# Kernel optimization log

Hardware: AMD Instinct MI355X
Metric: run time of the kernel (lower is better)

## Reference

```python
import jax, jax.numpy as jnp
import numpy as np

N = 50000      # nodes
E = 800000     # edges (before self loops)
IN = 128       # in_channels
C = 64         # out_channels per head
H = 4          # heads (both layers)
NEG_SLOPE = 0.2


def setup_inputs():
    key = jax.random.key(0)
    ks = jax.random.split(key, 14)
    nrm = lambda k, sh, s: jax.random.normal(k, sh, dtype=jnp.float32) * s
    x = nrm(ks[0], (N, IN), 1.0)
    edge_index = jax.random.randint(ks[1], (2, E), 0, N, dtype=jnp.int32)
    batch = jnp.zeros((N,), dtype=jnp.int32)
    edge_attr = jax.random.uniform(ks[2], (E, 1), dtype=jnp.float32)
    # layer 1 params (PyG GATConv: lin, att_src, att_dst, lin_edge, att_edge, bias)
    W1 = nrm(ks[3], (IN, H * C), 1.0 / np.sqrt(IN))
    We1 = nrm(ks[4], (1, H * C), 1.0)
    att_s1 = nrm(ks[5], (H, C), 1.0 / np.sqrt(C))
    att_d1 = nrm(ks[6], (H, C), 1.0 / np.sqrt(C))
    att_e1 = nrm(ks[7], (H, C), 1.0 / np.sqrt(C))
    b1 = jnp.zeros((H * C,), dtype=jnp.float32)
    # layer 2 params (in = H*C = 256)
    W2 = nrm(ks[8], (H * C, H * C), 1.0 / np.sqrt(H * C))
    We2 = nrm(ks[9], (1, H * C), 1.0)
    att_s2 = nrm(ks[10], (H, C), 1.0 / np.sqrt(C))
    att_d2 = nrm(ks[11], (H, C), 1.0 / np.sqrt(C))
    att_e2 = nrm(ks[12], (H, C), 1.0 / np.sqrt(C))
    b2 = jnp.zeros((H * C,), dtype=jnp.float32)
    return dict(x=x, edge_index=edge_index, batch=batch, edge_attr=edge_attr,
                W1=W1, We1=We1, att_s1=att_s1, att_d1=att_d1, att_e1=att_e1, b1=b1,
                W2=W2, We2=We2, att_s2=att_s2, att_d2=att_d2, att_e2=att_e2, b2=b2)


def gat_layer(h_in, src, dst, e_attr, W, We, att_s, att_d, att_e, b):
    n = h_in.shape[0]
    h = (h_in @ W).reshape(n, H, C)                      # [N,H,C]
    a_src = jnp.einsum('nhc,hc->nh', h, att_s)           # [N,H]
    a_dst = jnp.einsum('nhc,hc->nh', h, att_d)
    e = (e_attr @ We).reshape(-1, H, C)                  # [E',H,C]
    a_edge = jnp.einsum('ehc,hc->eh', e, att_e)          # [E',H]
    alpha = jax.nn.leaky_relu(a_src[src] + a_dst[dst] + a_edge, NEG_SLOPE)
    # softmax over edges grouped by destination node
    amax = jax.ops.segment_max(alpha, dst, num_segments=n)
    amax = jnp.where(jnp.isfinite(amax), amax, 0.0)
    ex = jnp.exp(alpha - amax[dst])
    denom = jax.ops.segment_sum(ex, dst, num_segments=n)
    a = ex / (denom[dst] + 1e-16)                        # [E',H]
    out = jax.ops.segment_sum(a[:, :, None] * h[src], dst, num_segments=n)
    return out.reshape(n, H * C) + b


def reference(x, edge_index, batch, edge_attr,
              W1, We1, att_s1, att_d1, att_e1, b1,
              W2, We2, att_s2, att_d2, att_e2, b2):
    n = x.shape[0]
    # PyG GATConv default: add self loops, self-loop edge_attr = mean fill
    loop = jnp.arange(n, dtype=edge_index.dtype)
    src = jnp.concatenate([edge_index[0], loop])
    dst = jnp.concatenate([edge_index[1], loop])
    ea_fill = jnp.broadcast_to(edge_attr.mean(axis=0, keepdims=True), (n, edge_attr.shape[1]))
    ea = jnp.concatenate([edge_attr, ea_fill], axis=0)
    h1 = gat_layer(x, src, dst, ea, W1, We1, att_s1, att_d1, att_e1, b1)
    h2 = gat_layer(h1, src, dst, ea, W2, We2, att_s2, att_d2, att_e2, b2)
    return h2
```

## Files before the change

kernel.cpp:

```cpp
#include <hip/hip_runtime.h>

#define NEG_SLOPE 0.2f

typedef __attribute__((ext_vector_type(8))) short bf16x8;
typedef __attribute__((ext_vector_type(4))) float f32x4;

__device__ inline unsigned short f2bf(float x) {
  unsigned int u = __float_as_uint(x);
  u += 0x7fffu + ((u >> 16) & 1u);
  return (unsigned short)(u >> 16);
}

__device__ inline unsigned fkey(float x) {
  unsigned u = __float_as_uint(x);
  return (u >> 31) ? ~u : (u | 0x80000000u);
}
__device__ inline float fkey_dec(unsigned k) {
  unsigned u = (k & 0x80000000u) ? (k ^ 0x80000000u) : ~k;
  return __uint_as_float(u);
}


__global__ void hist_kernel(const int* __restrict__ ei, int* __restrict__ counts,
                            int E, int Etot) {
  int e = blockIdx.x * blockDim.x + threadIdx.x;
  if (e >= Etot) return;
  int d = (e < E) ? ei[E + e] : (e - E);
  atomicAdd(&counts[d], 1);
}

__global__ void mean_kernel(const float* __restrict__ ea, float* __restrict__ acc, int E) {
  int i = blockIdx.x * blockDim.x + threadIdx.x;
  float s = 0.f;
  for (; i < E; i += gridDim.x * blockDim.x) s += ea[i];
#pragma unroll
  for (int off = 1; off < 64; off <<= 1) s += __shfl_xor(s, off, 64);
  if ((threadIdx.x & 63) == 0) atomicAdd(acc, s);
}

__global__ void scan_blocksum(const int* __restrict__ counts, int* __restrict__ bsum, int Nn) {
  int base = blockIdx.x * 4096 + threadIdx.x * 16;
  int s = 0;
#pragma unroll
  for (int i = 0; i < 16; i++) { int idx = base + i; if (idx < Nn) s += counts[idx]; }
#pragma unroll
  for (int off = 1; off < 64; off <<= 1) s += __shfl_xor(s, off, 64);
  __shared__ int ws_[4];
  if ((threadIdx.x & 63) == 0) ws_[threadIdx.x >> 6] = s;
  __syncthreads();
  if (threadIdx.x == 0) bsum[blockIdx.x] = ws_[0] + ws_[1] + ws_[2] + ws_[3];
}

__global__ void scan_offsets(int* bsum, int nb, int* rowptrN,
                             const float* meanacc, float* meanv, int E) {
  if (threadIdx.x == 0 && blockIdx.x == 0) {
    int acc = 0;
    for (int i = 0; i < nb; i++) { int v = bsum[i]; bsum[i] = acc; acc += v; }
    *rowptrN = acc;
    *meanv = *meanacc / (float)E;
  }
}

__global__ void scan_final(const int* __restrict__ counts, const int* __restrict__ bsum,
                           int* __restrict__ rowptr, int* __restrict__ cursor, int Nn) {
  int base = blockIdx.x * 4096 + threadIdx.x * 16;
  int v[16]; int s = 0;
#pragma unroll
  for (int i = 0; i < 16; i++) { int idx = base + i; v[i] = (idx < Nn) ? counts[idx] : 0; s += v[i]; }
  int lane = threadIdx.x & 63, wv = threadIdx.x >> 6;
  int incl = s;
#pragma unroll
  for (int off = 1; off < 64; off <<= 1) {
    int y = __shfl_up(incl, off, 64);
    if (lane >= off) incl += y;
  }
  __shared__ int wtot[4];
  if (lane == 63) wtot[wv] = incl;
  __syncthreads();
  int run = bsum[blockIdx.x] + incl - s;
  for (int i = 0; i < wv; i++) run += wtot[i];
  for (int i = 0; i < 16; i++) {
    int idx = base + i;
    if (idx < Nn) { rowptr[idx] = run; cursor[idx] = run; }
    run += v[i];
  }
}

__global__ void scatter_kernel(const int* __restrict__ ei, const float* __restrict__ eattr,
                               const float* __restrict__ meanv,
                               int* __restrict__ cursor, int2* __restrict__ epack,
                               int E, int Etot) {
  int e = blockIdx.x * blockDim.x + threadIdx.x;
  if (e >= Etot) return;
  int d, s; float ea;
  if (e < E) { d = ei[E + e]; s = ei[e]; ea = eattr[e]; }
  else       { d = e - E;     s = e - E; ea = meanv[0]; }
  int pos = atomicAdd(&cursor[d], 1);
  epack[pos] = make_int2(s, __float_as_int(ea));
}

__global__ void weatt_kernel(const float* __restrict__ We1, const float* __restrict__ atte1,
                             const float* __restrict__ We2, const float* __restrict__ atte2,
                             float* __restrict__ weatt1, float* __restrict__ weatt2) {
  int t = threadIdx.x;
  const float* We = (t < 256) ? We1 : We2;
  const float* at = (t < 256) ? atte1 : atte2;
  float* wo = (t < 256) ? weatt1 : weatt2;
  int i = t & 255;
  float p = We[i] * at[i];
#pragma unroll
  for (int off = 1; off < 64; off <<= 1) p += __shfl_xor(p, off, 64);
  if ((i & 63) == 0) wo[i >> 6] = p;
}

__global__ void wtrans_kernel(const float* __restrict__ W1, unsigned short* __restrict__ Wt1,
                              const float* __restrict__ W2, unsigned short* __restrict__ Wt2) {
  int b = blockIdx.x;
  const float* W; unsigned short* Wt; int K, t;
  if (b < 128) { W = W1; Wt = Wt1; K = 128; t = b * 256 + threadIdx.x; }
  else         { W = W2; Wt = Wt2; K = 256; t = (b - 128) * 256 + threadIdx.x; }
  int n = t & 255, k = t >> 8;
  if (k >= K) return;
  Wt[(size_t)n * K + k] = f2bf(W[(size_t)k * 256 + n]);
}


template <int AF32>
__device__ inline bf16x8 load_a_row(const void* Ain, int gr, int K, int kpos, int M) {
  bf16x8 v = {};
  if (gr < M) {
    if (AF32) {
      const float* src = (const float*)Ain + (size_t)gr * K + kpos;
      float4 f0 = *(const float4*)src;
      float4 f1 = *(const float4*)(src + 4);
      v[0] = (short)f2bf(f0.x); v[1] = (short)f2bf(f0.y);
      v[2] = (short)f2bf(f0.z); v[3] = (short)f2bf(f0.w);
      v[4] = (short)f2bf(f1.x); v[5] = (short)f2bf(f1.y);
      v[6] = (short)f2bf(f1.z); v[7] = (short)f2bf(f1.w);
    } else {
      v = *(const bf16x8*)((const unsigned short*)Ain + (size_t)gr * K + kpos);
    }
  }
  return v;
}

#define CS_STRIDE 264

template <int AF32>
__global__ __launch_bounds__(512) void gemm_att(const void* __restrict__ Ain,
                                                const unsigned short* __restrict__ Wt,
                                                unsigned short* __restrict__ Hb,
                                                const float* __restrict__ atts,
                                                const float* __restrict__ attd,
                                                float* __restrict__ asrc,
                                                float* __restrict__ adst,
                                                unsigned* __restrict__ gmaxk,
                                                int M, int K) {
  __shared__ __align__(16) short smem[(128 + 256) * 64];
  short* As = smem;
  short* Bs = smem + 128 * 64;
  short* Cs = smem;
  const int tid = threadIdx.x;
  const int lane = tid & 63, wv = tid >> 6;
  const int wm = wv >> 2, wn = wv & 3;
  const int l15 = lane & 15, l4 = lane >> 4;
  const int bm = blockIdx.x * 128;

  const int r0 = tid >> 3, kc = (tid & 7) * 8;
  const int nbB = tid >> 3, cB = (tid & 7) * 8;

  f32x4 acc[4][4] = {};
  bf16x8 ra0, ra1, rb0, rb1, rb2, rb3;

#define GLOAD_TILE(K0, A0, A1, B0, B1, B2, B3)                                 \
  {                                                                            \
    A0 = load_a_row<AF32>(Ain, bm + r0, K, (K0) + kc, M);                      \
    A1 = load_a_row<AF32>(Ain, bm + r0 + 64, K, (K0) + kc, M);                 \
    B0 = *(const bf16x8*)&Wt[(size_t)(nbB +   0) * K + (K0) + cB];             \
    B1 = *(const bf16x8*)&Wt[(size_t)(nbB +  64) * K + (K0) + cB];             \
    B2 = *(const bf16x8*)&Wt[(size_t)(nbB + 128) * K + (K0) + cB];             \
    B3 = *(const bf16x8*)&Wt[(size_t)(nbB + 192) * K + (K0) + cB];             \
  }

  GLOAD_TILE(0, ra0, ra1, rb0, rb1, rb2, rb3)

  for (int k0 = 0; k0 < K; k0 += 64) {
    *(bf16x8*)&As[((r0) * 64 + kc) ^ ((r0 & 7) << 3)] = ra0;
    *(bf16x8*)&As[((r0 + 64) * 64 + kc) ^ ((r0 & 7) << 3)] = ra1;
    *(bf16x8*)&Bs[((nbB) * 64 + cB) ^ ((nbB & 7) << 3)] = rb0;
    *(bf16x8*)&Bs[((nbB + 64) * 64 + cB) ^ ((nbB & 7) << 3)] = rb1;
    *(bf16x8*)&Bs[((nbB + 128) * 64 + cB) ^ ((nbB & 7) << 3)] = rb2;
    *(bf16x8*)&Bs[((nbB + 192) * 64 + cB) ^ ((nbB & 7) << 3)] = rb3;
    __syncthreads();

    bool more = (k0 + 64 < K);
    bf16x8 na0, na1, nb0, nb1, nb2, nb3;
    if (more) GLOAD_TILE(k0 + 64, na0, na1, nb0, nb1, nb2, nb3)

    bf16x8 af[4][2], bfr[4][2];
#pragma unroll
    for (int rt = 0; rt < 4; rt++)
#pragma unroll
      for (int ks = 0; ks < 2; ks++) {
        int row = wm * 64 + rt * 16 + l15;
        int kb = l4 * 8 + ks * 32;
        af[rt][ks] = *(const bf16x8*)&As[(row * 64 + kb) ^ ((row & 7) << 3)];
      }
#pragma unroll
    for (int ct = 0; ct < 4; ct++)
#pragma unroll
      for (int ks = 0; ks < 2; ks++) {
        int n = wn * 64 + ct * 16 + l15;
        int kb = l4 * 8 + ks * 32;
        bfr[ct][ks] = *(const bf16x8*)&Bs[(n * 64 + kb) ^ ((n & 7) << 3)];
      }
#pragma unroll
    for (int rt = 0; rt < 4; rt++)
#pragma unroll
      for (int ct = 0; ct < 4; ct++)
#pragma unroll
        for (int ks = 0; ks < 2; ks++)
          acc[rt][ct] = __builtin_amdgcn_mfma_f32_16x16x32_bf16(
              af[rt][ks], bfr[ct][ks], acc[rt][ct], 0, 0, 0);
    __syncthreads();

    if (more) { ra0 = na0; ra1 = na1; rb0 = nb0; rb1 = nb1; rb2 = nb2; rb3 = nb3; }
  }
#undef GLOAD_TILE

  float s_att[4], d_att[4];
#pragma unroll
  for (int ct = 0; ct < 4; ct++) {
    s_att[ct] = atts[wn * 64 + ct * 16 + l15];
    d_att[ct] = attd[wn * 64 + ct * 16 + l15];
  }
  float ps[4][4] = {}, pd[4][4] = {};
#pragma unroll
  for (int rt = 0; rt < 4; rt++)
#pragma unroll
    for (int ct = 0; ct < 4; ct++)
#pragma unroll
      for (int i = 0; i < 4; i++) {
        float v = acc[rt][ct][i];
        ps[rt][i] = fmaf(v, s_att[ct], ps[rt][i]);
        pd[rt][i] = fmaf(v, d_att[ct], pd[rt][i]);
      }

  for (int h = 0; h < 2; h++) {
    __syncthreads();
    if (wm == h) {
#pragma unroll
      for (int rt = 0; rt < 4; rt++)
#pragma unroll
        for (int ct = 0; ct < 4; ct++)
#pragma unroll
          for (int i = 0; i < 4; i++) {
            int lrow = rt * 16 + l4 * 4 + i;
            Cs[lrow * CS_STRIDE + wn * 64 + ct * 16 + l15] = f2bf(acc[rt][ct][i]);
          }
    }
    __syncthreads();
    int row = tid >> 3, seg = tid & 7;
    int gr = bm + h * 64 + row;
    if (gr < M) {
      const short* srcr = &Cs[row * CS_STRIDE + seg * 32];
      unsigned short* dstr = &Hb[(size_t)gr * 256 + seg * 32];
#pragma unroll
      for (int k = 0; k < 4; k++)
        *(uint4*)&dstr[k * 8] = *(const uint4*)&srcr[k * 8];
    }
  }

#pragma unroll
  for (int rt = 0; rt < 4; rt++)
#pragma unroll
    for (int i = 0; i < 4; i++) {
#pragma unroll
      for (int off = 1; off < 16; off <<= 1) {
        ps[rt][i] += __shfl_xor(ps[rt][i], off, 64);
        pd[rt][i] += __shfl_xor(pd[rt][i], off, 64);
      }
    }
  float mx = ps[0][0];
#pragma unroll
  for (int rt = 0; rt < 4; rt++)
#pragma unroll
    for (int i = 0; i < 4; i++) mx = fmaxf(mx, ps[rt][i]);
  mx = fmaxf(mx, __shfl_xor(mx, 16, 64));
  mx = fmaxf(mx, __shfl_xor(mx, 32, 64));
  if (lane == 0) atomicMax(&gmaxk[wn * 32], fkey(mx));
  if (l15 == 0) {
#pragma unroll
    for (int rt = 0; rt < 4; rt++)
#pragma unroll
      for (int i = 0; i < 4; i++) {
        int gr = bm + wm * 64 + rt * 16 + l4 * 4 + i;
        if (gr < M) {
          asrc[gr * 4 + wn] = ps[rt][i];
          adst[gr * 4 + wn] = pd[rt][i];
        }
      }
  }
}


#define AGG_PH1(CNT)                                                        \
  int src = 0; float w = 0.f;                                               \
  if (il < (CNT)) {                                                         \
    int2 e = epack[p + il];                                                 \
    float al = fmaf(__int_as_float(e.y), wa, asrc[e.x * 4 + hh] + ad);      \
    al = fmaxf(al, NEG_SLOPE * al);                                         \
    w = __expf(al - b);                                                     \
    src = e.x;                                                              \
  }                                                                         \
  ssum += w;

#define AGG_GATHER(i)                                                       \
  {                                                                         \
    int sl = (i) | hb16;                                                    \
    int si = __shfl(src, sl, 64);                                           \
    float wi = __shfl(w, sl, 64);                                           \
    uint2 hv = *(const uint2*)&Hb[(size_t)((unsigned)si * 256u + co)];      \
    acc.x = fmaf(wi, __uint_as_float(hv.x << 16), acc.x);                   \
    acc.y = fmaf(wi, __uint_as_float(hv.x & 0xffff0000u), acc.y);           \
    acc.z = fmaf(wi, __uint_as_float(hv.y << 16), acc.z);                   \
    acc.w = fmaf(wi, __uint_as_float(hv.y & 0xffff0000u), acc.w);           \
  }

template <int OUTBF>
__global__ __launch_bounds__(256) void gat_agg(const unsigned short* __restrict__ Hb,
                                               const float* __restrict__ asrc,
                                               const float* __restrict__ adst,
                                               const int* __restrict__ rowptr,
                                               const int2* __restrict__ epack,
                                               const float* __restrict__ weatt,
                                               const unsigned* __restrict__ gmaxk,
                                               const float* __restrict__ bias,
                                               unsigned short* __restrict__ outb,
                                               float* __restrict__ outf, int Nn) {
  int wid = (blockIdx.x * blockDim.x + threadIdx.x) >> 6;
  int lane = threadIdx.x & 63;
  if (wid >= Nn) return;
  int beg = rowptr[wid], end = rowptr[wid + 1];
  int hh = lane >> 4;
  int il = lane & 15;
  int hb16 = lane & 48;
  float wa = weatt[hh];
  float ad = adst[wid * 4 + hh];
  float braw = ad + fkey_dec(gmaxk[hh * 32]) + fmaxf(wa, 0.f);
  float b = fmaxf(braw, NEG_SLOPE * braw);
  unsigned co = (unsigned)lane * 4u;

  float ssum = 0.f;
  float4 acc = {0.f, 0.f, 0.f, 0.f};

  int p = beg;
  for (; p + 16 <= end; p += 16) {
    AGG_PH1(16)
#pragma unroll
    for (int i = 0; i < 16; i++) AGG_GATHER(i)
  }
  int cnt = end - p;
  if (cnt > 0) {
    AGG_PH1(cnt)
    for (int i = 0; i < cnt; i++) AGG_GATHER(i)
  }

#pragma unroll
  for (int off = 1; off < 16; off <<= 1) ssum += __shfl_xor(ssum, off, 64);

  float inv = 1.f / (ssum + 1e-16f);
  float4 b4 = *(const float4*)&bias[co];
  float4 r;
  r.x = fmaf(acc.x, inv, b4.x);
  r.y = fmaf(acc.y, inv, b4.y);
  r.z = fmaf(acc.z, inv, b4.z);
  r.w = fmaf(acc.w, inv, b4.w);
  if (OUTBF) {
    unsigned lo = (unsigned)f2bf(r.x) | ((unsigned)f2bf(r.y) << 16);
    unsigned hi = (unsigned)f2bf(r.z) | ((unsigned)f2bf(r.w) << 16);
    *(uint2*)&outb[(size_t)wid * 256 + co] = make_uint2(lo, hi);
  } else {
    *(float4*)&outf[(size_t)wid * 256 + co] = r;
  }
}


extern "C" void kernel_launch(void* const* d_in, const int* in_sizes, int n_in,
                              void* d_out, int out_size, void* d_ws, size_t ws_size,
                              hipStream_t stream) {
  (void)n_in; (void)out_size; (void)ws_size;
  const float* x     = (const float*)d_in[0];
  const int*   ei    = (const int*)d_in[1];
  const float* eattr = (const float*)d_in[3];
  const float* W1    = (const float*)d_in[4];
  const float* We1   = (const float*)d_in[5];
  const float* atts1 = (const float*)d_in[6];
  const float* attd1 = (const float*)d_in[7];
  const float* atte1 = (const float*)d_in[8];
  const float* b1    = (const float*)d_in[9];
  const float* W2    = (const float*)d_in[10];
  const float* We2   = (const float*)d_in[11];
  const float* atts2 = (const float*)d_in[12];
  const float* attd2 = (const float*)d_in[13];
  const float* atte2 = (const float*)d_in[14];
  const float* b2    = (const float*)d_in[15];
  float* out = (float*)d_out;

  const int Nn   = in_sizes[0] / 128;
  const int E    = in_sizes[1] / 2;
  const int Etot = E + Nn;

  char* p = (char*)d_ws;
  auto alloc = [&](size_t bytes) { void* r = (void*)p; p += (bytes + 255) & ~(size_t)255; return r; };
  int*      counts  = (int*)alloc((size_t)Nn * 4);
  float*    meanacc = (float*)alloc(4);
  unsigned* gmaxk1  = (unsigned*)alloc(512);
  unsigned* gmaxk2  = (unsigned*)alloc(512);
  char* zero_end = p;
  int*   rowptr  = (int*)alloc((size_t)(Nn + 1) * 4);
  int*   cursor  = (int*)alloc((size_t)Nn * 4);
  int2*  epack   = (int2*)alloc((size_t)Etot * 8);
  int*   bsum    = (int*)alloc(64 * 4);
  float* meanv   = (float*)alloc(4);
  float* weatt1  = (float*)alloc(16);
  float* weatt2  = (float*)alloc(16);
  float* asrc    = (float*)alloc((size_t)Nn * 4 * 4);
  float* adst    = (float*)alloc((size_t)Nn * 4 * 4);
  unsigned short* hbuf = (unsigned short*)alloc((size_t)Nn * 256 * 2);
  unsigned short* h1b  = (unsigned short*)alloc((size_t)Nn * 256 * 2);
  unsigned short* Wt1  = (unsigned short*)alloc((size_t)256 * 128 * 2);
  unsigned short* Wt2  = (unsigned short*)alloc((size_t)256 * 256 * 2);

  const int NB = (Nn + 4095) / 4096;

  hipMemsetAsync(counts, 0, (size_t)(zero_end - (char*)counts), stream);

  hist_kernel<<<(Etot + 255) / 256, 256, 0, stream>>>(ei, counts, E, Etot);
  mean_kernel<<<512, 256, 0, stream>>>(eattr, meanacc, E);
  scan_blocksum<<<NB, 256, 0, stream>>>(counts, bsum, Nn);
  scan_offsets<<<1, 64, 0, stream>>>(bsum, NB, rowptr + Nn, meanacc, meanv, E);
  scan_final<<<NB, 256, 0, stream>>>(counts, bsum, rowptr, cursor, Nn);
  scatter_kernel<<<(Etot + 255) / 256, 256, 0, stream>>>(ei, eattr, meanv, cursor, epack, E, Etot);
  weatt_kernel<<<1, 512, 0, stream>>>(We1, atte1, We2, atte2, weatt1, weatt2);
  wtrans_kernel<<<384, 256, 0, stream>>>(W1, Wt1, W2, Wt2);

  const int gemmBlocks = (Nn + 127) / 128;
  const int nodeBlocks = (Nn + 3) / 4;

  gemm_att<1><<<gemmBlocks, 512, 0, stream>>>(x, Wt1, hbuf, atts1, attd1,
                                              asrc, adst, gmaxk1, Nn, 128);
  gat_agg<1><<<nodeBlocks, 256, 0, stream>>>(hbuf, asrc, adst, rowptr, epack,
                                             weatt1, gmaxk1, b1, h1b, nullptr, Nn);
  gemm_att<0><<<gemmBlocks, 512, 0, stream>>>(h1b, Wt2, hbuf, atts2, attd2,
                                              asrc, adst, gmaxk2, Nn, 256);
  gat_agg<0><<<nodeBlocks, 256, 0, stream>>>(hbuf, asrc, adst, rowptr, epack,
                                             weatt2, gmaxk2, b2, nullptr, out, Nn);
}
```

Baseline: 344.3 us.

## Merge scan kernels into single-block scan, fold weatt into wtrans, reduce gmax atomics

Replaces the three-kernel counts scan plus the mean finalisation with one 1024-thread single-block kernel, which also sums per-block mean partials instead of using a float atomic. The weatt computation is folded into an extra block of the weight-transpose kernel. In the GEMM, the attention-logit reduction moves before the C-tile store, and per-block max is combined in shared memory so only four atomics are issued per block. Together these cut kernel launches and atomic traffic, at the cost of a serial single-block scan over 50k counts.

```diff
diff --git a/kernel.cpp b/kernel.cpp
--- a/kernel.cpp
+++ b/kernel.cpp
@@ -29,60 +29,59 @@
   atomicAdd(&counts[d], 1);
 }
 
-__global__ void mean_kernel(const float* __restrict__ ea, float* __restrict__ acc, int E) {
+__global__ void mean_kernel(const float* __restrict__ ea, float* __restrict__ part, int E) {
   int i = blockIdx.x * blockDim.x + threadIdx.x;
   float s = 0.f;
   for (; i < E; i += gridDim.x * blockDim.x) s += ea[i];
 #pragma unroll
   for (int off = 1; off < 64; off <<= 1) s += __shfl_xor(s, off, 64);
-  if ((threadIdx.x & 63) == 0) atomicAdd(acc, s);
-}
-
-__global__ void scan_blocksum(const int* __restrict__ counts, int* __restrict__ bsum, int Nn) {
-  int base = blockIdx.x * 4096 + threadIdx.x * 16;
-  int s = 0;
-#pragma unroll
-  for (int i = 0; i < 16; i++) { int idx = base + i; if (idx < Nn) s += counts[idx]; }
-#pragma unroll
-  for (int off = 1; off < 64; off <<= 1) s += __shfl_xor(s, off, 64);
-  __shared__ int ws_[4];
+  __shared__ float ws_[4];
   if ((threadIdx.x & 63) == 0) ws_[threadIdx.x >> 6] = s;
   __syncthreads();
-  if (threadIdx.x == 0) bsum[blockIdx.x] = ws_[0] + ws_[1] + ws_[2] + ws_[3];
-}
-
-__global__ void scan_offsets(int* bsum, int nb, int* rowptrN,
-                             const float* meanacc, float* meanv, int E) {
-  if (threadIdx.x == 0 && blockIdx.x == 0) {
-    int acc = 0;
-    for (int i = 0; i < nb; i++) { int v = bsum[i]; bsum[i] = acc; acc += v; }
-    *rowptrN = acc;
-    *meanv = *meanacc / (float)E;
-  }
-}
-
-__global__ void scan_final(const int* __restrict__ counts, const int* __restrict__ bsum,
-                           int* __restrict__ rowptr, int* __restrict__ cursor, int Nn) {
-  int base = blockIdx.x * 4096 + threadIdx.x * 16;
-  int v[16]; int s = 0;
-#pragma unroll
-  for (int i = 0; i < 16; i++) { int idx = base + i; v[i] = (idx < Nn) ? counts[idx] : 0; s += v[i]; }
-  int lane = threadIdx.x & 63, wv = threadIdx.x >> 6;
+  if (threadIdx.x == 0) part[blockIdx.x] = ws_[0] + ws_[1] + ws_[2] + ws_[3];
+}
+
+__global__ __launch_bounds__(1024) void scan_all(const int* __restrict__ counts,
+                                                 int* __restrict__ rowptr,
+                                                 int* __restrict__ cursor,
+                                                 const float* __restrict__ meanpart,
+                                                 float* __restrict__ meanv,
+                                                 int Nn, int E, int npart) {
+  __shared__ int wsum[16];
+  __shared__ float fsum[16];
+  int t = threadIdx.x, lane = t & 63, wv = t >> 6;
+  float f = (t < npart) ? meanpart[t] : 0.f;
+#pragma unroll
+  for (int off = 1; off < 64; off <<= 1) f += __shfl_xor(f, off, 64);
+  if (lane == 0) fsum[wv] = f;
+  const int CH = (Nn + 1023) >> 10;
+  int base = t * CH;
+  int lim = base + CH < Nn ? base + CH : Nn;
+  int s = 0;
+  for (int i = base; i < lim; i++) s += counts[i];
   int incl = s;
 #pragma unroll
   for (int off = 1; off < 64; off <<= 1) {
     int y = __shfl_up(incl, off, 64);
     if (lane >= off) incl += y;
   }
-  __shared__ int wtot[4];
-  if (lane == 63) wtot[wv] = incl;
+  if (lane == 63) wsum[wv] = incl;
   __syncthreads();
-  int run = bsum[blockIdx.x] + incl - s;
-  for (int i = 0; i < wv; i++) run += wtot[i];
-  for (int i = 0; i < 16; i++) {
-    int idx = base + i;
-    if (idx < Nn) { rowptr[idx] = run; cursor[idx] = run; }
-    run += v[i];
+  if (t == 0) {
+    int acc = 0;
+    for (int i = 0; i < 16; i++) { int x = wsum[i]; wsum[i] = acc; acc += x; }
+    rowptr[Nn] = acc;
+    float fa = 0.f;
+    for (int i = 0; i < 16; i++) fa += fsum[i];
+    *meanv = fa / (float)E;
+  }
+  __syncthreads();
+  int run = wsum[wv] + incl - s;
+  for (int i = base; i < lim; i++) {
+    int c = counts[i];
+    rowptr[i] = run;
+    cursor[i] = run;
+    run += c;
   }
 }
 
@@ -99,23 +98,26 @@
   epack[pos] = make_int2(s, __float_as_int(ea));
 }
 
-__global__ void weatt_kernel(const float* __restrict__ We1, const float* __restrict__ atte1,
-                             const float* __restrict__ We2, const float* __restrict__ atte2,
-                             float* __restrict__ weatt1, float* __restrict__ weatt2) {
-  int t = threadIdx.x;
-  const float* We = (t < 256) ? We1 : We2;
-  const float* at = (t < 256) ? atte1 : atte2;
-  float* wo = (t < 256) ? weatt1 : weatt2;
-  int i = t & 255;
-  float p = We[i] * at[i];
-#pragma unroll
-  for (int off = 1; off < 64; off <<= 1) p += __shfl_xor(p, off, 64);
-  if ((i & 63) == 0) wo[i >> 6] = p;
-}
-
 __global__ void wtrans_kernel(const float* __restrict__ W1, unsigned short* __restrict__ Wt1,
-                              const float* __restrict__ W2, unsigned short* __restrict__ Wt2) {
+                              const float* __restrict__ W2, unsigned short* __restrict__ Wt2,
+                              const float* __restrict__ We1, const float* __restrict__ atte1,
+                              const float* __restrict__ We2, const float* __restrict__ atte2,
+                              float* __restrict__ weatt1, float* __restrict__ weatt2) {
   int b = blockIdx.x;
+  if (b >= 384) {
+    int i = threadIdx.x;
+#pragma unroll
+    for (int l = 0; l < 2; l++) {
+      const float* We = l ? We2 : We1;
+      const float* at = l ? atte2 : atte1;
+      float* wo = l ? weatt2 : weatt1;
+      float p = We[i] * at[i];
+#pragma unroll
+      for (int off = 1; off < 64; off <<= 1) p += __shfl_xor(p, off, 64);
+      if ((i & 63) == 0) wo[i >> 6] = p;
+    }
+    return;
+  }
   const float* W; unsigned short* Wt; int K, t;
   if (b < 128) { W = W1; Wt = Wt1; K = 128; t = b * 256 + threadIdx.x; }
   else         { W = W2; Wt = Wt2; K = 256; t = (b - 128) * 256 + threadIdx.x; }
@@ -157,6 +159,7 @@
                                                 unsigned* __restrict__ gmaxk,
                                                 int M, int K) {
   __shared__ __align__(16) short smem[(128 + 256) * 64];
+  __shared__ float gmx[8];
   short* As = smem;
   short* Bs = smem + 128 * 64;
   short* Cs = smem;
@@ -245,6 +248,37 @@
         ps[rt][i] = fmaf(v, s_att[ct], ps[rt][i]);
         pd[rt][i] = fmaf(v, d_att[ct], pd[rt][i]);
       }
+
+#pragma unroll
+  for (int rt = 0; rt < 4; rt++)
+#pragma unroll
+    for (int i = 0; i < 4; i++) {
+#pragma unroll
+      for (int off = 1; off < 16; off <<= 1) {
+        ps[rt][i] += __shfl_xor(ps[rt][i], off, 64);
+        pd[rt][i] += __shfl_xor(pd[rt][i], off, 64);
+      }
+    }
+  float mx = ps[0][0];
+#pragma unroll
+  for (int rt = 0; rt < 4; rt++)
+#pragma unroll
+    for (int i = 0; i < 4; i++) mx = fmaxf(mx, ps[rt][i]);
+  mx = fmaxf(mx, __shfl_xor(mx, 16, 64));
+  mx = fmaxf(mx, __shfl_xor(mx, 32, 64));
+  if (lane == 0) gmx[wv] = mx;
+  if (l15 == 0) {
+#pragma unroll
+    for (int rt = 0; rt < 4; rt++)
+#pragma unroll
+      for (int i = 0; i < 4; i++) {
+        int gr = bm + wm * 64 + rt * 16 + l4 * 4 + i;
+        if (gr < M) {
+          asrc[gr * 4 + wn] = ps[rt][i];
+          adst[gr * 4 + wn] = pd[rt][i];
+        }
+      }
+  }
 
   for (int h = 0; h < 2; h++) {
     __syncthreads();
@@ -271,35 +305,9 @@
     }
   }
 
-#pragma unroll
-  for (int rt = 0; rt < 4; rt++)
-#pragma unroll
-    for (int i = 0; i < 4; i++) {
-#pragma unroll
-      for (int off = 1; off < 16; off <<= 1) {
-        ps[rt][i] += __shfl_xor(ps[rt][i], off, 64);
-        pd[rt][i] += __shfl_xor(pd[rt][i], off, 64);
-      }
-    }
-  float mx = ps[0][0];
-#pragma unroll
-  for (int rt = 0; rt < 4; rt++)
-#pragma unroll
-    for (int i = 0; i < 4; i++) mx = fmaxf(mx, ps[rt][i]);
-  mx = fmaxf(mx, __shfl_xor(mx, 16, 64));
-  mx = fmaxf(mx, __shfl_xor(mx, 32, 64));
-  if (lane == 0) atomicMax(&gmaxk[wn * 32], fkey(mx));
-  if (l15 == 0) {
-#pragma unroll
-    for (int rt = 0; rt < 4; rt++)
-#pragma unroll
-      for (int i = 0; i < 4; i++) {
-        int gr = bm + wm * 64 + rt * 16 + l4 * 4 + i;
-        if (gr < M) {
-          asrc[gr * 4 + wn] = ps[rt][i];
-          adst[gr * 4 + wn] = pd[rt][i];
-        }
-      }
+  if (wv < 4 && lane == 0) {
+    float m2 = fmaxf(gmx[wv], gmx[wv + 4]);
+    atomicMax(&gmaxk[wv * 32], fkey(m2));
   }
 }
 
@@ -414,14 +422,13 @@
   char* p = (char*)d_ws;
   auto alloc = [&](size_t bytes) { void* r = (void*)p; p += (bytes + 255) & ~(size_t)255; return r; };
   int*      counts  = (int*)alloc((size_t)Nn * 4);
-  float*    meanacc = (float*)alloc(4);
   unsigned* gmaxk1  = (unsigned*)alloc(512);
   unsigned* gmaxk2  = (unsigned*)alloc(512);
   char* zero_end = p;
   int*   rowptr  = (int*)alloc((size_t)(Nn + 1) * 4);
   int*   cursor  = (int*)alloc((size_t)Nn * 4);
   int2*  epack   = (int2*)alloc((size_t)Etot * 8);
-  int*   bsum    = (int*)alloc(64 * 4);
+  float* meanpart= (float*)alloc(512 * 4);
   float* meanv   = (float*)alloc(4);
   float* weatt1  = (float*)alloc(16);
   float* weatt2  = (float*)alloc(16);
@@ -432,18 +439,14 @@
   unsigned short* Wt1  = (unsigned short*)alloc((size_t)256 * 128 * 2);
   unsigned short* Wt2  = (unsigned short*)alloc((size_t)256 * 256 * 2);
 
-  const int NB = (Nn + 4095) / 4096;
-
   hipMemsetAsync(counts, 0, (size_t)(zero_end - (char*)counts), stream);
 
   hist_kernel<<<(Etot + 255) / 256, 256, 0, stream>>>(ei, counts, E, Etot);
-  mean_kernel<<<512, 256, 0, stream>>>(eattr, meanacc, E);
-  scan_blocksum<<<NB, 256, 0, stream>>>(counts, bsum, Nn);
-  scan_offsets<<<1, 64, 0, stream>>>(bsum, NB, rowptr + Nn, meanacc, meanv, E);
-  scan_final<<<NB, 256, 0, stream>>>(counts, bsum, rowptr, cursor, Nn);
+  mean_kernel<<<512, 256, 0, stream>>>(eattr, meanpart, E);
+  scan_all<<<1, 1024, 0, stream>>>(counts, rowptr, cursor, meanpart, meanv, Nn, E, 512);
   scatter_kernel<<<(Etot + 255) / 256, 256, 0, stream>>>(ei, eattr, meanv, cursor, epack, E, Etot);
-  weatt_kernel<<<1, 512, 0, stream>>>(We1, atte1, We2, atte2, weatt1, weatt2);
-  wtrans_kernel<<<384, 256, 0, stream>>>(W1, Wt1, W2, Wt2);
+  wtrans_kernel<<<385, 256, 0, stream>>>(W1, Wt1, W2, Wt2, We1, atte1, We2, atte2,
+                                         weatt1, weatt2);
 
   const int gemmBlocks = (Nn + 127) / 128;
   const int nodeBlocks = (Nn + 3) / 4;
```

Result: slower. 408.6 us (+18.7%).
